# Optimization experiments

Hardware: AMD Instinct MI355X
Metric: run time of the kernel (lower is better)

The kernel has to match this reference:

```python
import jax, jax.numpy as jnp
import numpy as np

KSIZE = 5
KNUM = 16
STRIDE = 1


def setup_inputs() -> dict:
    key = jax.random.key(0)
    k1, k2 = jax.random.split(key, 2)
    mu_in = jax.random.normal(k1, (16, 28, 28, 1), dtype=jnp.float32)
    # w_mu init: normal(0, 0.05); w_sigma init: constant -2.2 (as in build())
    w_mu = 0.05 * jax.random.normal(k2, (KSIZE, KSIZE, 1, KNUM), dtype=jnp.float32)
    w_sigma = jnp.full((KNUM,), -2.2, dtype=jnp.float32)
    return {"mu_in": mu_in, "w_mu": w_mu, "w_sigma": w_sigma}


def reference(mu_in, w_mu, w_sigma):
    # mu path: standard NHWC conv, VALID padding
    mu_out = jax.lax.conv_general_dilated(
        mu_in, w_mu, window_strides=(STRIDE, STRIDE), padding='VALID',
        dimension_numbers=('NHWC', 'HWIO', 'NHWC'))

    # Sigma path: extract patches -> [B, P, F] matrix (patch ordering is a
    # permutation of TF's, which leaves the Gram matrix X X^T invariant)
    patches = jax.lax.conv_general_dilated_patches(
        mu_in, filter_shape=(KSIZE, KSIZE), window_strides=(STRIDE, STRIDE),
        padding='VALID', dimension_numbers=('NHWC', 'HWIO', 'NHWC'))
    B = mu_in.shape[0]
    X = patches.reshape(B, -1, patches.shape[-1])          # [B, P, F]
    G = jnp.einsum('bpf,bqf->bpq', X, X)                   # [B, P, P]

    # per-output-channel softplus scale, broadcast to [B, P, P, KNUM]
    scale = jnp.log1p(jnp.exp(w_sigma))                    # log(1 + exp(w_sigma))
    Sigma = scale * G[..., None]                           # [B, P, P, KNUM]

    Sigma = jnp.where(jnp.isnan(Sigma), jnp.zeros_like(Sigma), Sigma)
    Sigma = jnp.where(jnp.isinf(Sigma), jnp.zeros_like(Sigma), Sigma)

    # tf.linalg.set_diag acts on the LAST TWO dims -> [P, KNUM] matrices:
    # abs the entries Sigma[:, :, i, i] for i < min(P, KNUM)
    m = min(Sigma.shape[-2], Sigma.shape[-1])
    i = jnp.arange(m)
    Sigma = Sigma.at[..., i, i].set(jnp.abs(Sigma[..., i, i]))
    return (mu_out, Sigma)
```

## Files before the change

### kernel.cpp

```cpp
#include <hip/hip_runtime.h>
#include <math.h>

#define BATCH 16
#define H     28
#define W     28
#define KS    5
#define KN    16
#define OHW   24
#define P     576
#define NTHR  256
#define MU_OUT_ELEMS (BATCH * P * KN)

typedef float vfloat4 __attribute__((ext_vector_type(4)));

__global__ __launch_bounds__(NTHR) void vdp_fused_kernel(
    const float* __restrict__ mu_in,
    const float* __restrict__ w_mu,
    const float* __restrict__ w_sigma,
    float* __restrict__ out)
{
    __shared__ float mu_s[H * W];
    __shared__ float wmu_s[KS * KS * KN];
    __shared__ float sp_s[KN];

    const int tid  = threadIdx.x;
    const int wave = tid >> 6;
    const int lane = tid & 63;

    const int blocks_per_b = P / 4;
    const int b = blockIdx.x / blocks_per_b;
    const int p = (blockIdx.x % blocks_per_b) * 4 + wave;

    const float* mu_b = mu_in + b * (H * W);
    for (int i = tid; i < H * W; i += NTHR) mu_s[i] = mu_b[i];
    for (int i = tid; i < KS * KS * KN; i += NTHR) wmu_s[i] = w_mu[i];
    if (tid < KN) sp_s[tid] = log1pf(expf(w_sigma[tid]));
    __syncthreads();

    const int ph = p / OHW;
    const int pw = p % OHW;

    float Xp[KS * KS];
    #pragma unroll
    for (int kh = 0; kh < KS; ++kh)
        #pragma unroll
        for (int kw = 0; kw < KS; ++kw)
            Xp[kh * KS + kw] = mu_s[(ph + kh) * W + (pw + kw)];

    if (lane < KN) {
        float acc = 0.f;
        #pragma unroll
        for (int j = 0; j < KS * KS; ++j)
            acc += Xp[j] * wmu_s[j * KN + lane];
        out[(b * P + p) * KN + lane] = acc;
    }

    const int c = lane & 3;
    const float sc0 = sp_s[4 * c + 0];
    const float sc1 = sp_s[4 * c + 1];
    const float sc2 = sp_s[4 * c + 2];
    const float sc3 = sp_s[4 * c + 3];

    vfloat4* rowp = (vfloat4*)(out + MU_OUT_ELEMS + (size_t)(b * P + p) * (P * KN));

    float g[9];
    #pragma unroll
    for (int r = 0; r < 9; ++r) {
        const int q  = r * 64 + lane;
        const int qh = q / OHW;
        const int qw = q % OHW;
        const float* mq = &mu_s[qh * W + qw];
        float acc = 0.f;
        #pragma unroll
        for (int kh = 0; kh < KS; ++kh)
            #pragma unroll
            for (int kw = 0; kw < KS; ++kw)
                acc += Xp[kh * KS + kw] * mq[kh * W + kw];
        g[r] = acc;
    }

    float gq[36];
    #pragma unroll
    for (int s = 0; s < 36; ++s)
        gq[s] = __shfl(g[s >> 2], 16 * (s & 3) + (lane >> 2));

    #pragma unroll
    for (int s = 0; s < 36; ++s) {
        vfloat4 v = { gq[s] * sc0, gq[s] * sc1, gq[s] * sc2, gq[s] * sc3 };
        if (s == 0) {
            const int qq = lane >> 2;
            if ((qq >> 2) == c) {
                const int r2 = qq & 3;
                v[r2] = fabsf(v[r2]);
            }
        }
        rowp[s * 64 + lane] = v;
    }
}

extern "C" void kernel_launch(void* const* d_in, const int* in_sizes, int n_in,
                              void* d_out, int out_size, void* d_ws, size_t ws_size,
                              hipStream_t stream) {
    const float* mu_in   = (const float*)d_in[0];
    const float* w_mu    = (const float*)d_in[1];
    const float* w_sigma = (const float*)d_in[2];
    float* out = (float*)d_out;

    dim3 grid(BATCH * P / 4);
    dim3 block(NTHR);
    vdp_fused_kernel<<<grid, block, 0, stream>>>(mu_in, w_mu, w_sigma, out);
}
```

Before: 346.3 us.

## Split Gram computation and channel broadcast into two kernels via workspace

```diff
diff --git a/kernel.cpp b/kernel.cpp
--- a/kernel.cpp
+++ b/kernel.cpp
@@ -8,10 +8,99 @@
 #define KN    16
 #define OHW   24
 #define P     576
+#define PP    (P * P)
 #define NTHR  256
 #define MU_OUT_ELEMS (BATCH * P * KN)
+#define G_ELEMS      (BATCH * PP)
+#define SIG_F4       (BATCH * PP * KN / 4)
 
 typedef float vfloat4 __attribute__((ext_vector_type(4)));
+
+__global__ __launch_bounds__(NTHR) void gram_kernel(
+    const float* __restrict__ mu_in,
+    const float* __restrict__ w_mu,
+    float* __restrict__ G,
+    float* __restrict__ out)
+{
+    __shared__ float mu_s[H * W];
+    __shared__ float wmu_s[KS * KS * KN];
+
+    const int tid  = threadIdx.x;
+    const int wave = tid >> 6;
+    const int lane = tid & 63;
+
+    const int blocks_per_b = P / 4;
+    const int b = blockIdx.x / blocks_per_b;
+    const int p = (blockIdx.x % blocks_per_b) * 4 + wave;
+
+    const float* mu_b = mu_in + b * (H * W);
+    for (int i = tid; i < H * W; i += NTHR) mu_s[i] = mu_b[i];
+    for (int i = tid; i < KS * KS * KN; i += NTHR) wmu_s[i] = w_mu[i];
+    __syncthreads();
+
+    const int ph = p / OHW;
+    const int pw = p % OHW;
+
+    float Xp[KS * KS];
+    #pragma unroll
+    for (int kh = 0; kh < KS; ++kh)
+        #pragma unroll
+        for (int kw = 0; kw < KS; ++kw)
+            Xp[kh * KS + kw] = mu_s[(ph + kh) * W + (pw + kw)];
+
+    if (lane < KN) {
+        float acc = 0.f;
+        #pragma unroll
+        for (int j = 0; j < KS * KS; ++j)
+            acc += Xp[j] * wmu_s[j * KN + lane];
+        out[(b * P + p) * KN + lane] = acc;
+    }
+
+    float* grow = G + (size_t)(b * P + p) * P;
+    #pragma unroll
+    for (int r = 0; r < 9; ++r) {
+        const int q  = r * 64 + lane;
+        const int qh = q / OHW;
+        const int qw = q % OHW;
+        const float* mq = &mu_s[qh * W + qw];
+        float acc = 0.f;
+        #pragma unroll
+        for (int kh = 0; kh < KS; ++kh)
+            #pragma unroll
+            for (int kw = 0; kw < KS; ++kw)
+                acc += Xp[kh * KS + kw] * mq[kh * W + kw];
+        grow[q] = acc;
+    }
+}
+
+__global__ __launch_bounds__(NTHR) void bcast_kernel(
+    const float* __restrict__ G,
+    const float* __restrict__ w_sigma,
+    float* __restrict__ out)
+{
+    const int tid0 = (int)(blockIdx.x * NTHR + threadIdx.x);
+    const int S    = (int)(gridDim.x * NTHR);
+    const unsigned c = (unsigned)(tid0 & 3);
+
+    const float sc0 = log1pf(expf(w_sigma[4 * c + 0]));
+    const float sc1 = log1pf(expf(w_sigma[4 * c + 1]));
+    const float sc2 = log1pf(expf(w_sigma[4 * c + 2]));
+    const float sc3 = log1pf(expf(w_sigma[4 * c + 3]));
+
+    vfloat4* sig = (vfloat4*)(out + MU_OUT_ELEMS);
+
+    for (int F = tid0; F < SIG_F4; F += S) {
+        const unsigned idx = (unsigned)F >> 2;
+        const float g = G[idx];
+        vfloat4 v = { g * sc0, g * sc1, g * sc2, g * sc3 };
+        const unsigned q = idx % (unsigned)P;
+        if ((q >> 2) == c) {
+            const unsigned j = q & 3;
+            v[j] = fabsf(v[j]);
+        }
+        sig[F] = v;
+    }
+}
 
 __global__ __launch_bounds__(NTHR) void vdp_fused_kernel(
     const float* __restrict__ mu_in,
@@ -106,7 +195,15 @@
     const float* w_sigma = (const float*)d_in[2];
     float* out = (float*)d_out;
 
-    dim3 grid(BATCH * P / 4);
-    dim3 block(NTHR);
-    vdp_fused_kernel<<<grid, block, 0, stream>>>(mu_in, w_mu, w_sigma, out);
-}
+    const size_t g_bytes = (size_t)G_ELEMS * sizeof(float);
+    if (d_ws != nullptr && ws_size >= g_bytes) {
+        float* G = (float*)d_ws;
+        gram_kernel<<<dim3(BATCH * P / 4), dim3(NTHR), 0, stream>>>(
+            mu_in, w_mu, G, out);
+        bcast_kernel<<<dim3(768), dim3(NTHR), 0, stream>>>(
+            G, w_sigma, out);
+    } else {
+        vdp_fused_kernel<<<dim3(BATCH * P / 4), dim3(NTHR), 0, stream>>>(
+            mu_in, w_mu, w_sigma, out);
+    }
+}
```

Measured after the change: 384.5 us. 1.11x slower.
